# Kernel optimization log

Hardware: AMD Instinct MI355X
Metric: run time of the kernel (lower is better)

## Reference

```python
import jax, jax.numpy as jnp
import numpy as np

N, E = 50000, 800000
C_IN, C_OUT, HID = 64, 64, 64


def setup_inputs() -> dict:
    key = jax.random.key(0)
    ks = jax.random.split(key, 12)
    def rn(k, shape, scale=0.05):
        return jax.random.normal(k, shape, dtype=jnp.float32) * scale
    return dict(
        x=jax.random.normal(ks[0], (N, C_IN), dtype=jnp.float32),
        pos=jax.random.normal(ks[1], (N, 3), dtype=jnp.float32),
        edge_index=jax.random.randint(ks[2], (2, E), 0, N),
        W_in=rn(ks[3], (C_IN, C_IN)), b_in=jnp.zeros((C_IN,), jnp.float32),
        W_out=rn(ks[4], (C_OUT, C_OUT)), b_out=jnp.zeros((C_OUT,), jnp.float32),
        W_lin=rn(ks[5], (C_OUT, C_IN)),   # PointTransformerConv.lin (value), bias=False
        W_src=rn(ks[6], (C_OUT, C_IN)),   # lin_src, bias=False
        W_dst=rn(ks[7], (C_OUT, C_IN)),   # lin_dst, bias=False
        pos_w1=rn(ks[8], (HID, 3)), pos_b1=jnp.zeros((HID,), jnp.float32),
        pos_w2=rn(ks[9], (C_OUT, HID)), pos_b2=jnp.zeros((C_OUT,), jnp.float32),
        att_w1=rn(ks[10], (HID, C_OUT)), att_b1=jnp.zeros((HID,), jnp.float32),
        att_w2=rn(ks[11], (C_OUT, HID)), att_b2=jnp.zeros((C_OUT,), jnp.float32),
    )


def _mlp2(y, w1, b1, w2, b2):
    # MLP([a, 64, b], batch_norm=False): Linear->ReLU->Linear->ReLU
    y = jax.nn.relu(y @ w1.T + b1)
    return jax.nn.relu(y @ w2.T + b2)


def reference(x, pos, edge_index, W_in, b_in, W_out, b_out, W_lin, W_src, W_dst,
              pos_w1, pos_b1, pos_w2, pos_b2, att_w1, att_b1, att_w2, att_b2):
    n = x.shape[0]
    h = jax.nn.relu(x @ W_in.T + b_in)            # lin_in + relu, (N, C_in)
    v = h @ W_lin.T                                # value projection (N, C_out)
    k_src = h @ W_src.T                            # alpha_j source part
    q_dst = h @ W_dst.T                            # alpha_i dest part
    # PointTransformerConv adds self-loops by default
    loop = jnp.arange(n)
    src = jnp.concatenate([edge_index[0], loop])   # (E+N,)
    dst = jnp.concatenate([edge_index[1], loop])
    # per-edge positional encoding: pos_nn(pos_i - pos_j)
    delta = _mlp2(pos[dst] - pos[src], pos_w1, pos_b1, pos_w2, pos_b2)
    # per-edge attention logits: attn_nn(alpha_i - alpha_j), (E+N, C_out)
    alpha = _mlp2(q_dst[dst] - k_src[src], att_w1, att_b1, att_w2, att_b2)
    # per-destination-node channelwise softmax (self-loops ensure no empty segment)
    amax = jax.ops.segment_max(alpha, dst, num_segments=n)
    ex = jnp.exp(alpha - amax[dst])
    denom = jax.ops.segment_sum(ex, dst, num_segments=n)
    w = ex / (denom[dst] + 1e-16)
    # message = alpha * (x_j + delta); aggregate = sum over neighbors
    out = jax.ops.segment_sum(w * (v[src] + delta), dst, num_segments=n)
    return jax.nn.relu(out @ W_out.T + b_out)
```

## Files before the change

kernel.cpp:

```cpp
#include <hip/hip_runtime.h>
#include <math.h>

#define NN 50000
#define EE 800000
#define ET (EE + NN)
#define C  64
#define NBLK 49
#define NCHUNK 831
#define ZBLK 463

typedef __attribute__((ext_vector_type(8))) _Float16 f16x8;
typedef __attribute__((ext_vector_type(4))) _Float16 f16x4;
typedef __attribute__((ext_vector_type(2))) _Float16 f16x2;
typedef __attribute__((ext_vector_type(4))) float f32x4;

__device__ __forceinline__ f16x2 pk2(float a, float b) {
  return __builtin_bit_cast(f16x2, __builtin_amdgcn_cvt_pkrtz(a, b));
}
__device__ __forceinline__ f16x4 pk4(float a, float b, float c, float d) {
  return __builtin_shufflevector(pk2(a, b), pk2(c, d), 0, 1, 2, 3);
}
__device__ __forceinline__ f16x8 pk8(const float* y) {
  const f16x4 lo = pk4(y[0], y[1], y[2], y[3]);
  const f16x4 hi = pk4(y[4], y[5], y[6], y[7]);
  return __builtin_shufflevector(lo, hi, 0, 1, 2, 3, 4, 5, 6, 7);
}

__device__ __forceinline__ f16x8 frag_ldh(const _Float16* base, int row,
                                          int kofs) {
  return *(const f16x8*)(base + row * 72 + kofs);
}

__device__ __forceinline__ void stage_w(_Float16* __restrict__ dst,
                                        const _Float16* __restrict__ src16,
                                        int tid) {
  const f16x8* src = (const f16x8*)(src16 + tid * 16);
  _Float16* d = dst + (tid >> 2) * 72 + (tid & 3) * 16;
  ((f16x8*)d)[0] = src[0];
  ((f16x8*)d)[1] = src[1];
}

__global__ __launch_bounds__(256) void prep_kernel(
    const float* __restrict__ W_in, const float* __restrict__ W_lin,
    const float* __restrict__ W_src, const float* __restrict__ W_dst,
    const float* __restrict__ att_w1, const float* __restrict__ att_w2,
    const float* __restrict__ pos_w2, const float* __restrict__ W_out,
    _Float16* __restrict__ w16, int* __restrict__ cnt2) {
  const float* Ws[8] = {W_in, W_lin, W_src, W_dst, att_w1, att_w2, pos_w2, W_out};
  const float* src = Ws[blockIdx.x];
  _Float16* dst = w16 + blockIdx.x * 4096;
#pragma unroll
  for (int i = threadIdx.x * 4; i < 4096; i += 1024) {
    const float4 w = *(const float4*)(src + i);
    *(f16x4*)(dst + i) = pk4(w.x, w.y, w.z, w.w);
  }
  int4* cz = (int4*)(cnt2 + blockIdx.x * NN);
#pragma unroll 1
  for (int i = threadIdx.x; i < NN / 4; i += 256) cz[i] = make_int4(0, 0, 0, 0);
}

__global__ __launch_bounds__(256) void scan_partial(const int* __restrict__ cnt2,
                                                    int* __restrict__ bsum,
                                                    float* __restrict__ zeroreg) {
  const int t = threadIdx.x;
  if (blockIdx.x >= NBLK) {
    const int zb = blockIdx.x - NBLK;
    float4* dst = (float4*)zeroreg;
    const int total4 = 2 * NN * 64 / 4;
    const float4 z = make_float4(0.f, 0.f, 0.f, 0.f);
#pragma unroll 1
    for (int i = zb * 256 + t; i < total4; i += ZBLK * 256) dst[i] = z;
    return;
  }
  __shared__ int ws[4];
  const int base = blockIdx.x * 1024 + t * 4;
  int s = 0;
  if (base + 3 < NN) {
#pragma unroll
    for (int sh = 0; sh < 8; ++sh) {
      const int4 v = *(const int4*)(cnt2 + sh * NN + base);
      s += v.x + v.y + v.z + v.w;
    }
  } else {
#pragma unroll
    for (int i = 0; i < 4; ++i)
      if (base + i < NN)
#pragma unroll
        for (int sh = 0; sh < 8; ++sh) s += cnt2[sh * NN + base + i];
  }
#pragma unroll
  for (int off = 32; off; off >>= 1) s += __shfl_down(s, off, 64);
  if ((t & 63) == 0) ws[t >> 6] = s;
  __syncthreads();
  if (t == 0) bsum[blockIdx.x] = ws[0] + ws[1] + ws[2] + ws[3];
}

__global__ __launch_bounds__(256) void scan_final(const int* __restrict__ cnt2,
                                                  const int* __restrict__ bsum,
                                                  int* __restrict__ curs2) {
  __shared__ int tsum[256];
  __shared__ int sblk[64];
  const int t = threadIdx.x;
  if (t < 64) {
    const int mine = (t < NBLK) ? bsum[t] : 0;
    int v = mine;
#pragma unroll
    for (int off = 1; off < 64; off <<= 1) {
      const int u = __shfl_up(v, off, 64);
      if (t >= off) v += u;
    }
    sblk[t] = v - mine;
  }
  const int base = blockIdx.x * 1024 + t * 4;
  int c2[8][4];
  int v[4] = {0, 0, 0, 0};
  if (base + 3 < NN) {
#pragma unroll
    for (int sh = 0; sh < 8; ++sh) {
      const int4 x = *(const int4*)(cnt2 + sh * NN + base);
      c2[sh][0] = x.x; c2[sh][1] = x.y; c2[sh][2] = x.z; c2[sh][3] = x.w;
      v[0] += x.x; v[1] += x.y; v[2] += x.z; v[3] += x.w;
    }
  } else {
#pragma unroll
    for (int sh = 0; sh < 8; ++sh)
#pragma unroll
      for (int i = 0; i < 4; ++i) {
        const int c = (base + i < NN) ? cnt2[sh * NN + base + i] : 0;
        c2[sh][i] = c;
        v[i] += c;
      }
  }
  const int s = v[0] + v[1] + v[2] + v[3];
  tsum[t] = s;
  __syncthreads();
  for (int off = 1; off < 256; off <<= 1) {
    const int u = (t >= off) ? tsum[t - off] : 0;
    __syncthreads();
    tsum[t] += u;
    __syncthreads();
  }
  int ex = sblk[blockIdx.x] + tsum[t] - s;
  int offs[8][4];
#pragma unroll
  for (int i = 0; i < 4; ++i) {
    int run = ex;
#pragma unroll
    for (int sh = 0; sh < 8; ++sh) {
      offs[sh][i] = run;
      run += c2[sh][i];
    }
    ex += v[i];
  }
  if (base + 3 < NN) {
#pragma unroll
    for (int sh = 0; sh < 8; ++sh)
      *(int4*)(curs2 + sh * NN + base) =
          make_int4(offs[sh][0], offs[sh][1], offs[sh][2], offs[sh][3]);
  } else {
#pragma unroll
    for (int sh = 0; sh < 8; ++sh)
#pragma unroll
      for (int i = 0; i < 4; ++i)
        if (base + i < NN) curs2[sh * NN + base + i] = offs[sh][i];
  }
}

__global__ void scatter_kernel(const int* __restrict__ ei,
                               int* __restrict__ curs2, int2* __restrict__ srt) {
  const int chunk = blockIdx.x;
  int* cs = curs2 + (chunk & 7) * NN;
  const int e0 = chunk * 1024 + threadIdx.x * 4;
  if (e0 >= ET) return;
  int s[4], d[4];
  if (e0 + 3 < EE) {
    const int4 sv = *(const int4*)(ei + e0);
    const int4 dv = *(const int4*)(ei + EE + e0);
    s[0] = sv.x; s[1] = sv.y; s[2] = sv.z; s[3] = sv.w;
    d[0] = dv.x; d[1] = dv.y; d[2] = dv.z; d[3] = dv.w;
  } else {
#pragma unroll
    for (int i = 0; i < 4; ++i) {
      const int e = e0 + i;
      if (e < EE) {
        s[i] = ei[e];
        d[i] = ei[EE + e];
      } else if (e < ET) {
        s[i] = d[i] = e - EE;
      } else {
        s[i] = d[i] = -1;
      }
    }
  }
#pragma unroll
  for (int i = 0; i < 4; ++i) {
    if (d[i] >= 0) {
      const int p = atomicAdd(&cs[d[i]], 1);
      srt[p] = make_int2(s[i], d[i]);
    }
  }
}

__global__ __launch_bounds__(256, 3) void node_proj(
    const float* __restrict__ x, const float* __restrict__ b_in,
    const _Float16* __restrict__ w16, const int* __restrict__ ei,
    int* __restrict__ cnt2, _Float16* __restrict__ vh,
    _Float16* __restrict__ kh, _Float16* __restrict__ qh) {
  __shared__ __align__(16) _Float16 wlds[4 * 4608];
  __shared__ __align__(16) _Float16 hlds[4608];
  __shared__ float biasv[64];

  const int tid = threadIdx.x;
  const int nb = blockIdx.x * 64;
  const int l15 = tid & 15;
  const int quad = (tid >> 4) & 3;
  const int wband = tid >> 6;
  const int nloc = wband * 16 + l15;
  const int gn = nb + nloc;

#pragma unroll 1
  for (int chunk = blockIdx.x; chunk < NCHUNK; chunk += gridDim.x) {
    int* cs = cnt2 + (chunk & 7) * NN;
    const int e0 = chunk * 1024 + tid * 4;
    if (e0 < ET) {
      int d[4];
      if (e0 + 3 < EE) {
        const int4 dv = *(const int4*)(ei + EE + e0);
        d[0] = dv.x; d[1] = dv.y; d[2] = dv.z; d[3] = dv.w;
      } else {
#pragma unroll
        for (int i = 0; i < 4; ++i) {
          const int e = e0 + i;
          d[i] = (e < EE) ? ei[EE + e] : ((e < ET) ? e - EE : -1);
        }
      }
#pragma unroll
      for (int i = 0; i < 4; ++i)
        if (d[i] >= 0) atomicAdd(&cs[d[i]], 1);
    }
  }

#pragma unroll
  for (int w = 0; w < 4; ++w) stage_w(wlds + w * 4608, w16 + w * 4096, tid);
  if (tid < 64) biasv[tid] = b_in[tid];

  f16x8 bfrag[2];
#pragma unroll
  for (int ks = 0; ks < 2; ++ks) {
    float y[8] = {0.f, 0.f, 0.f, 0.f, 0.f, 0.f, 0.f, 0.f};
    if (gn < NN) {
      const float4 a = *(const float4*)(x + (size_t)gn * 64 + ks * 32 + quad * 8);
      const float4 b = *(const float4*)(x + (size_t)gn * 64 + ks * 32 + quad * 8 + 4);
      y[0] = a.x; y[1] = a.y; y[2] = a.z; y[3] = a.w;
      y[4] = b.x; y[5] = b.y; y[6] = b.z; y[7] = b.w;
    }
    bfrag[ks] = pk8(y);
  }
  __syncthreads();

#pragma unroll
  for (int t = 0; t < 4; ++t) {
    f32x4 acc = {0.f, 0.f, 0.f, 0.f};
#pragma unroll
    for (int ks = 0; ks < 2; ++ks) {
      const f16x8 af = frag_ldh(wlds, t * 16 + l15, ks * 32 + quad * 8);
      acc = __builtin_amdgcn_mfma_f32_16x16x32_f16(af, bfrag[ks], acc, 0, 0, 0);
    }
    const int hb = t * 16 + quad * 4;
    *(f16x4*)(hlds + nloc * 72 + hb) =
        pk4(fmaxf(acc[0] + biasv[hb + 0], 0.f), fmaxf(acc[1] + biasv[hb + 1], 0.f),
            fmaxf(acc[2] + biasv[hb + 2], 0.f), fmaxf(acc[3] + biasv[hb + 3], 0.f));
  }
  __syncthreads();

  f16x8 hfrag[2];
#pragma unroll
  for (int ks = 0; ks < 2; ++ks)
    hfrag[ks] = frag_ldh(hlds, nloc, ks * 32 + quad * 8);

  _Float16* outs[3] = {vh, kh, qh};
#pragma unroll
  for (int p = 0; p < 3; ++p) {
    const _Float16* W = wlds + (p + 1) * 4608;
#pragma unroll
    for (int t = 0; t < 4; ++t) {
      f32x4 acc = {0.f, 0.f, 0.f, 0.f};
#pragma unroll
      for (int ks = 0; ks < 2; ++ks) {
        const f16x8 af = frag_ldh(W, t * 16 + l15, ks * 32 + quad * 8);
        acc = __builtin_amdgcn_mfma_f32_16x16x32_f16(af, hfrag[ks], acc, 0, 0, 0);
      }
      if (gn < NN) {
        *(f16x4*)(outs[p] + (size_t)gn * 64 + t * 16 + quad * 4) =
            pk4(acc[0], acc[1], acc[2], acc[3]);
      }
    }
  }
}

__global__ __launch_bounds__(256, 4) void edge_pass(
    const int2* __restrict__ srt, const float* __restrict__ pos,
    const _Float16* __restrict__ vh, const _Float16* __restrict__ kh,
    const _Float16* __restrict__ qh, const _Float16* __restrict__ w16,
    const float* __restrict__ att_b1, const float* __restrict__ att_b2,
    const float* __restrict__ pos_w1, const float* __restrict__ pos_b1,
    const float* __restrict__ pos_b2, float* __restrict__ num,
    float* __restrict__ den) {
  __shared__ __align__(16) _Float16 smem[18432];
  __shared__ __align__(16) float posw1T[3 * 64];
  __shared__ float b1s[64], b2s[64], pb1s[64], pb2s[64];
  __shared__ int dsts[64];

  _Float16* W1  = smem;
  _Float16* W2  = smem + 4608;
  _Float16* PW2 = smem + 9216;
  _Float16* h1  = smem + 13824;
  float2* pairb = (float2*)smem;

  const int tid = threadIdx.x;
  const int eb = blockIdx.x * 64;
  const int l15 = tid & 15;
  const int quad = (tid >> 4) & 3;
  const int wband = tid >> 6;
  const int eloc = wband * 16 + l15;

  int s_mine, d_mine;
  f16x8 bfrag[2];
  float dp0, dp1, dp2;
  {
    const int e = eb + eloc;
    int2 sd = make_int2(0, 0);
    int valid_d = -1;
    if (e < ET) {
      sd = srt[e];
      valid_d = sd.y;
    }
    s_mine = sd.x;
    d_mine = sd.y;
    if (quad == 0) dsts[eloc] = valid_d;
#pragma unroll
    for (int ks = 0; ks < 2; ++ks) {
      const f16x8 qv =
          *(const f16x8*)(qh + (size_t)d_mine * 64 + ks * 32 + quad * 8);
      const f16x8 kv =
          *(const f16x8*)(kh + (size_t)s_mine * 64 + ks * 32 + quad * 8);
      bfrag[ks] = qv - kv;
    }
    dp0 = pos[(size_t)d_mine * 3 + 0] - pos[(size_t)s_mine * 3 + 0];
    dp1 = pos[(size_t)d_mine * 3 + 1] - pos[(size_t)s_mine * 3 + 1];
    dp2 = pos[(size_t)d_mine * 3 + 2] - pos[(size_t)s_mine * 3 + 2];
  }

  stage_w(W1, w16 + 4 * 4096, tid);
  stage_w(W2, w16 + 5 * 4096, tid);
  stage_w(PW2, w16 + 6 * 4096, tid);
  if (tid < 64) {
    b1s[tid] = att_b1[tid];
    b2s[tid] = att_b2[tid];
    pb1s[tid] = pos_b1[tid];
    pb2s[tid] = pos_b2[tid];
    posw1T[0 * 64 + tid] = pos_w1[tid * 3 + 0];
    posw1T[1 * 64 + tid] = pos_w1[tid * 3 + 1];
    posw1T[2 * 64 + tid] = pos_w1[tid * 3 + 2];
  }
  __syncthreads();

#pragma unroll
  for (int t = 0; t < 4; ++t) {
    f32x4 acc = {0.f, 0.f, 0.f, 0.f};
#pragma unroll
    for (int ks = 0; ks < 2; ++ks) {
      const f16x8 af = frag_ldh(W1, t * 16 + l15, ks * 32 + quad * 8);
      acc = __builtin_amdgcn_mfma_f32_16x16x32_f16(af, bfrag[ks], acc, 0, 0, 0);
    }
    const int hb = t * 16 + quad * 4;
    *(f16x4*)(h1 + eloc * 72 + hb) =
        pk4(fmaxf(acc[0] + b1s[hb + 0], 0.f), fmaxf(acc[1] + b1s[hb + 1], 0.f),
            fmaxf(acc[2] + b1s[hb + 2], 0.f), fmaxf(acc[3] + b1s[hb + 3], 0.f));
  }

  f16x8 hpfrag[2];
#pragma unroll
  for (int ks = 0; ks < 2; ++ks) {
    float hv[8];
#pragma unroll
    for (int j = 0; j < 8; ++j) {
      const int i = ks * 32 + quad * 8 + j;
      float a = pb1s[i];
      a = fmaf(dp0, posw1T[i], a);
      a = fmaf(dp1, posw1T[64 + i], a);
      a = fmaf(dp2, posw1T[128 + i], a);
      hv[j] = fmaxf(a, 0.f);
    }
    hpfrag[ks] = pk8(hv);
  }
  __syncthreads();

  float ex[16], del[16];
  {
    f16x8 hfrag[2];
#pragma unroll
    for (int ks = 0; ks < 2; ++ks)
      hfrag[ks] = frag_ldh(h1, eloc, ks * 32 + quad * 8);
#pragma unroll
    for (int t = 0; t < 4; ++t) {
      f32x4 acc = {0.f, 0.f, 0.f, 0.f};
#pragma unroll
      for (int ks = 0; ks < 2; ++ks) {
        const f16x8 af = frag_ldh(W2, t * 16 + l15, ks * 32 + quad * 8);
        acc = __builtin_amdgcn_mfma_f32_16x16x32_f16(af, hfrag[ks], acc, 0, 0, 0);
      }
      const int ob = t * 16 + quad * 4;
#pragma unroll
      for (int r = 0; r < 4; ++r)
        ex[t * 4 + r] = __expf(fmaxf(acc[r] + b2s[ob + r], 0.f));
    }
  }
#pragma unroll
  for (int t = 0; t < 4; ++t) {
    f32x4 acc = {0.f, 0.f, 0.f, 0.f};
#pragma unroll
    for (int ks = 0; ks < 2; ++ks) {
      const f16x8 af = frag_ldh(PW2, t * 16 + l15, ks * 32 + quad * 8);
      acc = __builtin_amdgcn_mfma_f32_16x16x32_f16(af, hpfrag[ks], acc, 0, 0, 0);
    }
    const int ob = t * 16 + quad * 4;
#pragma unroll
    for (int r = 0; r < 4; ++r)
      del[t * 4 + r] = fmaxf(acc[r] + pb2s[ob + r], 0.f);
  }
  float vr[16];
#pragma unroll
  for (int t = 0; t < 4; ++t) {
    const f16x4 v4 = *(const f16x4*)(vh + (size_t)s_mine * 64 + t * 16 + quad * 4);
    vr[t * 4 + 0] = (float)v4[0];
    vr[t * 4 + 1] = (float)v4[1];
    vr[t * 4 + 2] = (float)v4[2];
    vr[t * 4 + 3] = (float)v4[3];
  }
  __syncthreads();

#pragma unroll
  for (int t = 0; t < 4; ++t) {
#pragma unroll
    for (int r = 0; r < 4; ++r) {
      const int o = t * 16 + quad * 4 + r;
      const int sl = (eloc + 2 * o) & 63;
      const float e_ = ex[t * 4 + r];
      pairb[o * 65 + sl] = make_float2(e_ * (vr[t * 4 + r] + del[t * 4 + r]), e_);
    }
  }
  __syncthreads();

  {
    const int c = tid & 63;
    const int r = tid >> 6;
    float am = 0.f, ae = 0.f;
    int cur = -1;
#pragma unroll 1
    for (int t2 = 0; t2 < 16; ++t2) {
      const int el = r * 16 + t2;
      const int d = dsts[el];
      if (d != cur) {
        if (cur >= 0) {
          unsafeAtomicAdd(num + (size_t)cur * 64 + c, am);
          unsafeAtomicAdd(den + (size_t)cur * 64 + c, ae);
        }
        cur = d;
        am = 0.f;
        ae = 0.f;
      }
      if (d >= 0) {
        const float2 pe = pairb[c * 65 + ((el + 2 * c) & 63)];
        am += pe.x;
        ae += pe.y;
      }
    }
    if (cur >= 0) {
      unsafeAtomicAdd(num + (size_t)cur * 64 + c, am);
      unsafeAtomicAdd(den + (size_t)cur * 64 + c, ae);
    }
  }
}

__global__ __launch_bounds__(256, 4) void out_proj(
    const float* __restrict__ num, const float* __restrict__ den,
    const _Float16* __restrict__ w16, const float* __restrict__ b_out,
    float* __restrict__ out) {
  __shared__ __align__(16) _Float16 wlds[4608];
  __shared__ float biasv[64];

  const int tid = threadIdx.x;
  const int nb = blockIdx.x * 64;
  const int l15 = tid & 15;
  const int quad = (tid >> 4) & 3;
  const int wband = tid >> 6;
  const int gn = nb + wband * 16 + l15;

  stage_w(wlds, w16 + 7 * 4096, tid);
  if (tid < 64) biasv[tid] = b_out[tid];

  f16x8 bfrag[2];
#pragma unroll
  for (int ks = 0; ks < 2; ++ks) {
    float y[8] = {0.f, 0.f, 0.f, 0.f, 0.f, 0.f, 0.f, 0.f};
    if (gn < NN) {
      const size_t base = (size_t)gn * 64 + ks * 32 + quad * 8;
      const float4 n0 = *(const float4*)(num + base);
      const float4 n1 = *(const float4*)(num + base + 4);
      const float4 d0 = *(const float4*)(den + base);
      const float4 d1 = *(const float4*)(den + base + 4);
      y[0] = n0.x / (d0.x + 1e-16f); y[1] = n0.y / (d0.y + 1e-16f);
      y[2] = n0.z / (d0.z + 1e-16f); y[3] = n0.w / (d0.w + 1e-16f);
      y[4] = n1.x / (d1.x + 1e-16f); y[5] = n1.y / (d1.y + 1e-16f);
      y[6] = n1.z / (d1.z + 1e-16f); y[7] = n1.w / (d1.w + 1e-16f);
    }
    bfrag[ks] = pk8(y);
  }
  __syncthreads();

#pragma unroll
  for (int t = 0; t < 4; ++t) {
    f32x4 acc = {0.f, 0.f, 0.f, 0.f};
#pragma unroll
    for (int ks = 0; ks < 2; ++ks) {
      const f16x8 af = frag_ldh(wlds, t * 16 + l15, ks * 32 + quad * 8);
      acc = __builtin_amdgcn_mfma_f32_16x16x32_f16(af, bfrag[ks], acc, 0, 0, 0);
    }
    if (gn < NN) {
      const int ob = t * 16 + quad * 4;
      float4 r;
      r.x = fmaxf(acc[0] + biasv[ob + 0], 0.f);
      r.y = fmaxf(acc[1] + biasv[ob + 1], 0.f);
      r.z = fmaxf(acc[2] + biasv[ob + 2], 0.f);
      r.w = fmaxf(acc[3] + biasv[ob + 3], 0.f);
      *(float4*)(out + (size_t)gn * 64 + ob) = r;
    }
  }
}

extern "C" void kernel_launch(void* const* d_in, const int* in_sizes, int n_in,
                              void* d_out, int out_size, void* d_ws,
                              size_t ws_size, hipStream_t stream) {
  const float* x      = (const float*)d_in[0];
  const float* pos    = (const float*)d_in[1];
  const int*   ei     = (const int*)d_in[2];
  const float* W_in   = (const float*)d_in[3];
  const float* b_in   = (const float*)d_in[4];
  const float* W_out  = (const float*)d_in[5];
  const float* b_out  = (const float*)d_in[6];
  const float* W_lin  = (const float*)d_in[7];
  const float* W_src  = (const float*)d_in[8];
  const float* W_dst  = (const float*)d_in[9];
  const float* pos_w1 = (const float*)d_in[10];
  const float* pos_b1 = (const float*)d_in[11];
  const float* pos_w2 = (const float*)d_in[12];
  const float* pos_b2 = (const float*)d_in[13];
  const float* att_w1 = (const float*)d_in[14];
  const float* att_b1 = (const float*)d_in[15];
  const float* att_w2 = (const float*)d_in[16];
  const float* att_b2 = (const float*)d_in[17];

  float* ws = (float*)d_ws;
  const size_t NC = (size_t)NN * C;
  float* num = ws;
  float* den = ws + NC;
  _Float16* vh = (_Float16*)(ws + 2 * NC);
  _Float16* kh = vh + NC;
  _Float16* qh = kh + NC;
  _Float16* w16 = qh + NC;
  int* ib     = (int*)(w16 + 8 * 4096);
  int* cnt2   = ib;
  int* curs2  = ib + 8 * NN;
  int* bsum   = ib + 16 * NN;
  int2* srt   = (int2*)(((uintptr_t)(bsum + NBLK) + 15) & ~(uintptr_t)15);

  const dim3 blk(256);
  prep_kernel<<<dim3(8), blk, 0, stream>>>(W_in, W_lin, W_src, W_dst, att_w1,
                                           att_w2, pos_w2, W_out, w16, cnt2);
  node_proj<<<dim3((NN + 63) / 64), blk, 0, stream>>>(x, b_in, w16, ei, cnt2,
                                                      vh, kh, qh);
  scan_partial<<<dim3(NBLK + ZBLK), blk, 0, stream>>>(cnt2, bsum, num);
  scan_final<<<dim3(NBLK), blk, 0, stream>>>(cnt2, bsum, curs2);
  scatter_kernel<<<dim3(NCHUNK), blk, 0, stream>>>(ei, curs2, srt);
  edge_pass<<<dim3((ET + 63) / 64), blk, 0, stream>>>(
      srt, pos, vh, kh, qh, w16, att_b1, att_b2, pos_w1, pos_b1, pos_b2, num,
      den);
  out_proj<<<dim3((NN + 63) / 64), blk, 0, stream>>>(num, den, w16, b_out,
                                                     (float*)d_out);
}
```

Measured before the change: 307.3 us.

## Fuse all stages into one cooperative persistent kernel with grid syncs

Replaces the seven-kernel pipeline (prep, node projection, scan partial, scan final, scatter, edge pass, output projection) with a single cooperative persistent kernel. Stages are separated by grid-wide barriers and work is distributed over tiles in grid-stride loops. The aim is to remove per-launch overhead and inter-kernel gaps. In exchange it adds grid-sync cost and serializes the small scan stages on only 49 blocks. It also re-stages weights into LDS for every tile, and the original kernels remain as a fallback if the cooperative launch fails.

```diff
diff --git a/kernel.cpp b/kernel.cpp
--- a/kernel.cpp
+++ b/kernel.cpp
@@ -1,5 +1,8 @@
 #include <hip/hip_runtime.h>
+#include <hip/hip_cooperative_groups.h>
 #include <math.h>
+
+namespace cg = cooperative_groups;
 
 #define NN 50000
 #define EE 800000
@@ -8,6 +11,8 @@
 #define NBLK 49
 #define NCHUNK 831
 #define ZBLK 463
+#define NTILE 782
+#define ETILE 13282
 
 typedef __attribute__((ext_vector_type(8))) _Float16 f16x8;
 typedef __attribute__((ext_vector_type(4))) _Float16 f16x4;
@@ -38,6 +43,516 @@
   _Float16* d = dst + (tid >> 2) * 72 + (tid & 3) * 16;
   ((f16x8*)d)[0] = src[0];
   ((f16x8*)d)[1] = src[1];
+}
+
+struct MegaArgs {
+  const float *x, *pos;
+  const int* ei;
+  const float *W_in, *b_in, *W_out, *b_out, *W_lin, *W_src, *W_dst;
+  const float *pos_w1, *pos_b1, *pos_w2, *pos_b2;
+  const float *att_w1, *att_b1, *att_w2, *att_b2;
+  float *num, *den;
+  _Float16 *vh, *kh, *qh, *w16;
+  int *cnt2, *curs2, *bsum;
+  int2* srt;
+  float* out;
+};
+
+__global__ __launch_bounds__(256, 4) void mega_kernel(MegaArgs a) {
+  cg::grid_group grd = cg::this_grid();
+  __shared__ __align__(16) _Float16 smem[18432];
+  __shared__ __align__(16) float posw1T[192];
+  __shared__ float b1s[64], b2s[64], pb1s[64], pb2s[64];
+  __shared__ int dsts[64];
+
+  const int tid = threadIdx.x;
+  const int bid = blockIdx.x;
+  const int gsz = gridDim.x;
+  const int l15 = tid & 15;
+  const int quad = (tid >> 4) & 3;
+  const int wband = tid >> 6;
+
+  {
+    const int gt = bid * 256 + tid;
+    const int stride = gsz * 256;
+    float4* z1 = (float4*)a.num;
+    const float4 zf = make_float4(0.f, 0.f, 0.f, 0.f);
+#pragma unroll 1
+    for (int i = gt; i < (2 * NN * C) / 4; i += stride) z1[i] = zf;
+    int4* z2 = (int4*)a.cnt2;
+    const int4 zi = make_int4(0, 0, 0, 0);
+#pragma unroll 1
+    for (int i = gt; i < (8 * NN) / 4; i += stride) z2[i] = zi;
+    if (bid < 8) {
+      const float* Ws[8] = {a.W_in,   a.W_lin,  a.W_src,  a.W_dst,
+                            a.att_w1, a.att_w2, a.pos_w2, a.W_out};
+      const float* src = Ws[bid];
+      _Float16* dst = a.w16 + bid * 4096;
+#pragma unroll 1
+      for (int i = tid * 4; i < 4096; i += 1024) {
+        const float4 w = *(const float4*)(src + i);
+        *(f16x4*)(dst + i) = pk4(w.x, w.y, w.z, w.w);
+      }
+    }
+  }
+  grd.sync();
+
+  {
+#pragma unroll 1
+    for (int chunk = bid; chunk < NCHUNK; chunk += gsz) {
+      int* cs = a.cnt2 + (chunk & 7) * NN;
+      const int e0 = chunk * 1024 + tid * 4;
+      if (e0 < ET) {
+        int d[4];
+        if (e0 + 3 < EE) {
+          const int4 dv = *(const int4*)(a.ei + EE + e0);
+          d[0] = dv.x; d[1] = dv.y; d[2] = dv.z; d[3] = dv.w;
+        } else {
+#pragma unroll
+          for (int i = 0; i < 4; ++i) {
+            const int e = e0 + i;
+            d[i] = (e < EE) ? a.ei[EE + e] : ((e < ET) ? e - EE : -1);
+          }
+        }
+#pragma unroll
+        for (int i = 0; i < 4; ++i)
+          if (d[i] >= 0) atomicAdd(&cs[d[i]], 1);
+      }
+    }
+    _Float16* A = smem;
+    _Float16* B = smem + 4608;
+    _Float16* Cr = smem + 9216;
+    _Float16* D = smem + 13824;
+#pragma unroll 1
+    for (int tile = bid; tile < NTILE; tile += gsz) {
+      __syncthreads();
+      const int nloc = wband * 16 + l15;
+      const int gn = tile * 64 + nloc;
+      stage_w(A, a.w16 + 0 * 4096, tid);
+      stage_w(B, a.w16 + 1 * 4096, tid);
+      stage_w(Cr, a.w16 + 2 * 4096, tid);
+      if (tid < 64) b1s[tid] = a.b_in[tid];
+      f16x8 bfrag[2];
+#pragma unroll
+      for (int ks = 0; ks < 2; ++ks) {
+        float y[8] = {0.f, 0.f, 0.f, 0.f, 0.f, 0.f, 0.f, 0.f};
+        if (gn < NN) {
+          const size_t base = (size_t)gn * 64 + ks * 32 + quad * 8;
+          const float4 p = *(const float4*)(a.x + base);
+          const float4 q = *(const float4*)(a.x + base + 4);
+          y[0] = p.x; y[1] = p.y; y[2] = p.z; y[3] = p.w;
+          y[4] = q.x; y[5] = q.y; y[6] = q.z; y[7] = q.w;
+        }
+        bfrag[ks] = pk8(y);
+      }
+      __syncthreads();
+#pragma unroll
+      for (int t = 0; t < 4; ++t) {
+        f32x4 acc = {0.f, 0.f, 0.f, 0.f};
+#pragma unroll
+        for (int ks = 0; ks < 2; ++ks) {
+          const f16x8 af = frag_ldh(A, t * 16 + l15, ks * 32 + quad * 8);
+          acc = __builtin_amdgcn_mfma_f32_16x16x32_f16(af, bfrag[ks], acc, 0, 0, 0);
+        }
+        const int hb = t * 16 + quad * 4;
+        *(f16x4*)(D + nloc * 72 + hb) = pk4(
+            fmaxf(acc[0] + b1s[hb + 0], 0.f), fmaxf(acc[1] + b1s[hb + 1], 0.f),
+            fmaxf(acc[2] + b1s[hb + 2], 0.f), fmaxf(acc[3] + b1s[hb + 3], 0.f));
+      }
+      __syncthreads();
+      f16x8 hfrag[2];
+#pragma unroll
+      for (int ks = 0; ks < 2; ++ks)
+        hfrag[ks] = frag_ldh(D, nloc, ks * 32 + quad * 8);
+      stage_w(A, a.w16 + 3 * 4096, tid);
+      _Float16* outs2[2] = {a.vh, a.kh};
+      const _Float16* Ws2[2] = {B, Cr};
+#pragma unroll
+      for (int p = 0; p < 2; ++p) {
+#pragma unroll
+        for (int t = 0; t < 4; ++t) {
+          f32x4 acc = {0.f, 0.f, 0.f, 0.f};
+#pragma unroll
+          for (int ks = 0; ks < 2; ++ks) {
+            const f16x8 af = frag_ldh(Ws2[p], t * 16 + l15, ks * 32 + quad * 8);
+            acc = __builtin_amdgcn_mfma_f32_16x16x32_f16(af, hfrag[ks], acc, 0, 0, 0);
+          }
+          if (gn < NN)
+            *(f16x4*)(outs2[p] + (size_t)gn * 64 + t * 16 + quad * 4) =
+                pk4(acc[0], acc[1], acc[2], acc[3]);
+        }
+      }
+      __syncthreads();
+#pragma unroll
+      for (int t = 0; t < 4; ++t) {
+        f32x4 acc = {0.f, 0.f, 0.f, 0.f};
+#pragma unroll
+        for (int ks = 0; ks < 2; ++ks) {
+          const f16x8 af = frag_ldh(A, t * 16 + l15, ks * 32 + quad * 8);
+          acc = __builtin_amdgcn_mfma_f32_16x16x32_f16(af, hfrag[ks], acc, 0, 0, 0);
+        }
+        if (gn < NN)
+          *(f16x4*)(a.qh + (size_t)gn * 64 + t * 16 + quad * 4) =
+              pk4(acc[0], acc[1], acc[2], acc[3]);
+      }
+    }
+  }
+  grd.sync();
+
+  {
+    int* wsb = (int*)smem;
+#pragma unroll 1
+    for (int sb = bid; sb < NBLK; sb += gsz) {
+      __syncthreads();
+      const int base = sb * 1024 + tid * 4;
+      int s = 0;
+      if (base + 3 < NN) {
+#pragma unroll
+        for (int sh = 0; sh < 8; ++sh) {
+          const int4 v = *(const int4*)(a.cnt2 + sh * NN + base);
+          s += v.x + v.y + v.z + v.w;
+        }
+      } else {
+#pragma unroll
+        for (int i = 0; i < 4; ++i)
+          if (base + i < NN)
+#pragma unroll
+            for (int sh = 0; sh < 8; ++sh) s += a.cnt2[sh * NN + base + i];
+      }
+#pragma unroll
+      for (int off = 32; off; off >>= 1) s += __shfl_down(s, off, 64);
+      if ((tid & 63) == 0) wsb[tid >> 6] = s;
+      __syncthreads();
+      if (tid == 0) a.bsum[sb] = wsb[0] + wsb[1] + wsb[2] + wsb[3];
+    }
+  }
+  grd.sync();
+
+  {
+    int* tsum = (int*)smem;
+    int* sblk = ((int*)smem) + 256;
+#pragma unroll 1
+    for (int sb = bid; sb < NBLK; sb += gsz) {
+      __syncthreads();
+      if (tid < 64) {
+        const int mine = (tid < NBLK) ? a.bsum[tid] : 0;
+        int v = mine;
+#pragma unroll
+        for (int off = 1; off < 64; off <<= 1) {
+          const int u = __shfl_up(v, off, 64);
+          if (tid >= off) v += u;
+        }
+        sblk[tid] = v - mine;
+      }
+      const int base = sb * 1024 + tid * 4;
+      int c2[8][4];
+      int v[4] = {0, 0, 0, 0};
+      if (base + 3 < NN) {
+#pragma unroll
+        for (int sh = 0; sh < 8; ++sh) {
+          const int4 xx = *(const int4*)(a.cnt2 + sh * NN + base);
+          c2[sh][0] = xx.x; c2[sh][1] = xx.y; c2[sh][2] = xx.z; c2[sh][3] = xx.w;
+          v[0] += xx.x; v[1] += xx.y; v[2] += xx.z; v[3] += xx.w;
+        }
+      } else {
+#pragma unroll
+        for (int sh = 0; sh < 8; ++sh)
+#pragma unroll
+          for (int i = 0; i < 4; ++i) {
+            const int c = (base + i < NN) ? a.cnt2[sh * NN + base + i] : 0;
+            c2[sh][i] = c;
+            v[i] += c;
+          }
+      }
+      const int s = v[0] + v[1] + v[2] + v[3];
+      tsum[tid] = s;
+      __syncthreads();
+      for (int off = 1; off < 256; off <<= 1) {
+        const int u = (tid >= off) ? tsum[tid - off] : 0;
+        __syncthreads();
+        tsum[tid] += u;
+        __syncthreads();
+      }
+      int ex = sblk[sb] + tsum[tid] - s;
+      int offs[8][4];
+#pragma unroll
+      for (int i = 0; i < 4; ++i) {
+        int run = ex;
+#pragma unroll
+        for (int sh = 0; sh < 8; ++sh) {
+          offs[sh][i] = run;
+          run += c2[sh][i];
+        }
+        ex += v[i];
+      }
+      if (base + 3 < NN) {
+#pragma unroll
+        for (int sh = 0; sh < 8; ++sh)
+          *(int4*)(a.curs2 + sh * NN + base) =
+              make_int4(offs[sh][0], offs[sh][1], offs[sh][2], offs[sh][3]);
+      } else {
+#pragma unroll
+        for (int sh = 0; sh < 8; ++sh)
+#pragma unroll
+          for (int i = 0; i < 4; ++i)
+            if (base + i < NN) a.curs2[sh * NN + base + i] = offs[sh][i];
+      }
+    }
+  }
+  grd.sync();
+
+  {
+#pragma unroll 1
+    for (int chunk = bid; chunk < NCHUNK; chunk += gsz) {
+      int* cs = a.curs2 + (chunk & 7) * NN;
+      const int e0 = chunk * 1024 + tid * 4;
+      if (e0 < ET) {
+        int s[4], d[4];
+        if (e0 + 3 < EE) {
+          const int4 sv = *(const int4*)(a.ei + e0);
+          const int4 dv = *(const int4*)(a.ei + EE + e0);
+          s[0] = sv.x; s[1] = sv.y; s[2] = sv.z; s[3] = sv.w;
+          d[0] = dv.x; d[1] = dv.y; d[2] = dv.z; d[3] = dv.w;
+        } else {
+#pragma unroll
+          for (int i = 0; i < 4; ++i) {
+            const int e = e0 + i;
+            if (e < EE) {
+              s[i] = a.ei[e];
+              d[i] = a.ei[EE + e];
+            } else if (e < ET) {
+              s[i] = d[i] = e - EE;
+            } else {
+              s[i] = d[i] = -1;
+            }
+          }
+        }
+#pragma unroll
+        for (int i = 0; i < 4; ++i) {
+          if (d[i] >= 0) {
+            const int p = atomicAdd(&cs[d[i]], 1);
+            a.srt[p] = make_int2(s[i], d[i]);
+          }
+        }
+      }
+    }
+  }
+  grd.sync();
+
+  {
+    _Float16* W1 = smem;
+    _Float16* W2 = smem + 4608;
+    _Float16* PW2 = smem + 9216;
+    _Float16* h1 = smem + 13824;
+    float2* pairb = (float2*)smem;
+    if (tid < 64) {
+      b1s[tid] = a.att_b1[tid];
+      b2s[tid] = a.att_b2[tid];
+      pb1s[tid] = a.pos_b1[tid];
+      pb2s[tid] = a.pos_b2[tid];
+      posw1T[0 * 64 + tid] = a.pos_w1[tid * 3 + 0];
+      posw1T[1 * 64 + tid] = a.pos_w1[tid * 3 + 1];
+      posw1T[2 * 64 + tid] = a.pos_w1[tid * 3 + 2];
+    }
+    const int eloc = wband * 16 + l15;
+#pragma unroll 1
+    for (int tile = bid; tile < ETILE; tile += gsz) {
+      __syncthreads();
+      const int eb = tile * 64;
+      int s_mine, d_mine;
+      f16x8 bfrag[2];
+      float dp0, dp1, dp2;
+      {
+        const int e = eb + eloc;
+        int2 sd = make_int2(0, 0);
+        int valid_d = -1;
+        if (e < ET) {
+          sd = a.srt[e];
+          valid_d = sd.y;
+        }
+        s_mine = sd.x;
+        d_mine = sd.y;
+        if (quad == 0) dsts[eloc] = valid_d;
+#pragma unroll
+        for (int ks = 0; ks < 2; ++ks) {
+          const f16x8 qv =
+              *(const f16x8*)(a.qh + (size_t)d_mine * 64 + ks * 32 + quad * 8);
+          const f16x8 kv =
+              *(const f16x8*)(a.kh + (size_t)s_mine * 64 + ks * 32 + quad * 8);
+          bfrag[ks] = qv - kv;
+        }
+        dp0 = a.pos[(size_t)d_mine * 3 + 0] - a.pos[(size_t)s_mine * 3 + 0];
+        dp1 = a.pos[(size_t)d_mine * 3 + 1] - a.pos[(size_t)s_mine * 3 + 1];
+        dp2 = a.pos[(size_t)d_mine * 3 + 2] - a.pos[(size_t)s_mine * 3 + 2];
+      }
+      stage_w(W1, a.w16 + 4 * 4096, tid);
+      stage_w(W2, a.w16 + 5 * 4096, tid);
+      stage_w(PW2, a.w16 + 6 * 4096, tid);
+      __syncthreads();
+
+#pragma unroll
+      for (int t = 0; t < 4; ++t) {
+        f32x4 acc = {0.f, 0.f, 0.f, 0.f};
+#pragma unroll
+        for (int ks = 0; ks < 2; ++ks) {
+          const f16x8 af = frag_ldh(W1, t * 16 + l15, ks * 32 + quad * 8);
+          acc = __builtin_amdgcn_mfma_f32_16x16x32_f16(af, bfrag[ks], acc, 0, 0, 0);
+        }
+        const int hb = t * 16 + quad * 4;
+        *(f16x4*)(h1 + eloc * 72 + hb) = pk4(
+            fmaxf(acc[0] + b1s[hb + 0], 0.f), fmaxf(acc[1] + b1s[hb + 1], 0.f),
+            fmaxf(acc[2] + b1s[hb + 2], 0.f), fmaxf(acc[3] + b1s[hb + 3], 0.f));
+      }
+      f16x8 hpfrag[2];
+#pragma unroll
+      for (int ks = 0; ks < 2; ++ks) {
+        float hv[8];
+#pragma unroll
+        for (int j = 0; j < 8; ++j) {
+          const int i = ks * 32 + quad * 8 + j;
+          float h = pb1s[i];
+          h = fmaf(dp0, posw1T[i], h);
+          h = fmaf(dp1, posw1T[64 + i], h);
+          h = fmaf(dp2, posw1T[128 + i], h);
+          hv[j] = fmaxf(h, 0.f);
+        }
+        hpfrag[ks] = pk8(hv);
+      }
+      __syncthreads();
+      float ex[16], del[16];
+      {
+        f16x8 hfrag[2];
+#pragma unroll
+        for (int ks = 0; ks < 2; ++ks)
+          hfrag[ks] = frag_ldh(h1, eloc, ks * 32 + quad * 8);
+#pragma unroll
+        for (int t = 0; t < 4; ++t) {
+          f32x4 acc = {0.f, 0.f, 0.f, 0.f};
+#pragma unroll
+          for (int ks = 0; ks < 2; ++ks) {
+            const f16x8 af = frag_ldh(W2, t * 16 + l15, ks * 32 + quad * 8);
+            acc = __builtin_amdgcn_mfma_f32_16x16x32_f16(af, hfrag[ks], acc, 0, 0, 0);
+          }
+          const int ob = t * 16 + quad * 4;
+#pragma unroll
+          for (int r = 0; r < 4; ++r)
+            ex[t * 4 + r] = __expf(fmaxf(acc[r] + b2s[ob + r], 0.f));
+        }
+      }
+#pragma unroll
+      for (int t = 0; t < 4; ++t) {
+        f32x4 acc = {0.f, 0.f, 0.f, 0.f};
+#pragma unroll
+        for (int ks = 0; ks < 2; ++ks) {
+          const f16x8 af = frag_ldh(PW2, t * 16 + l15, ks * 32 + quad * 8);
+          acc = __builtin_amdgcn_mfma_f32_16x16x32_f16(af, hpfrag[ks], acc, 0, 0, 0);
+        }
+        const int ob = t * 16 + quad * 4;
+#pragma unroll
+        for (int r = 0; r < 4; ++r)
+          del[t * 4 + r] = fmaxf(acc[r] + pb2s[ob + r], 0.f);
+      }
+      float vr[16];
+#pragma unroll
+      for (int t = 0; t < 4; ++t) {
+        const f16x4 v4 =
+            *(const f16x4*)(a.vh + (size_t)s_mine * 64 + t * 16 + quad * 4);
+        vr[t * 4 + 0] = (float)v4[0];
+        vr[t * 4 + 1] = (float)v4[1];
+        vr[t * 4 + 2] = (float)v4[2];
+        vr[t * 4 + 3] = (float)v4[3];
+      }
+      __syncthreads();
+#pragma unroll
+      for (int t = 0; t < 4; ++t) {
+#pragma unroll
+        for (int r = 0; r < 4; ++r) {
+          const int o = t * 16 + quad * 4 + r;
+          const int sl = (eloc + 2 * o) & 63;
+          const float e_ = ex[t * 4 + r];
+          pairb[o * 65 + sl] =
+              make_float2(e_ * (vr[t * 4 + r] + del[t * 4 + r]), e_);
+        }
+      }
+      __syncthreads();
+      {
+        const int c = tid & 63;
+        const int r = tid >> 6;
+        float am = 0.f, ae = 0.f;
+        int cur = -1;
+#pragma unroll 1
+        for (int t2 = 0; t2 < 16; ++t2) {
+          const int el = r * 16 + t2;
+          const int d = dsts[el];
+          if (d != cur) {
+            if (cur >= 0) {
+              unsafeAtomicAdd(a.num + (size_t)cur * 64 + c, am);
+              unsafeAtomicAdd(a.den + (size_t)cur * 64 + c, ae);
+            }
+            cur = d;
+            am = 0.f;
+            ae = 0.f;
+          }
+          if (d >= 0) {
+            const float2 pe = pairb[c * 65 + ((el + 2 * c) & 63)];
+            am += pe.x;
+            ae += pe.y;
+          }
+        }
+        if (cur >= 0) {
+          unsafeAtomicAdd(a.num + (size_t)cur * 64 + c, am);
+          unsafeAtomicAdd(a.den + (size_t)cur * 64 + c, ae);
+        }
+      }
+    }
+  }
+  grd.sync();
+
+  {
+    __syncthreads();
+    stage_w(smem, a.w16 + 7 * 4096, tid);
+    if (tid < 64) b1s[tid] = a.b_out[tid];
+    __syncthreads();
+#pragma unroll 1
+    for (int tile = bid; tile < NTILE; tile += gsz) {
+      const int gn = tile * 64 + wband * 16 + l15;
+      f16x8 bfrag[2];
+#pragma unroll
+      for (int ks = 0; ks < 2; ++ks) {
+        float y[8] = {0.f, 0.f, 0.f, 0.f, 0.f, 0.f, 0.f, 0.f};
+        if (gn < NN) {
+          const size_t base = (size_t)gn * 64 + ks * 32 + quad * 8;
+          const float4 n0 = *(const float4*)(a.num + base);
+          const float4 n1 = *(const float4*)(a.num + base + 4);
+          const float4 d0 = *(const float4*)(a.den + base);
+          const float4 d1 = *(const float4*)(a.den + base + 4);
+          y[0] = n0.x / (d0.x + 1e-16f); y[1] = n0.y / (d0.y + 1e-16f);
+          y[2] = n0.z / (d0.z + 1e-16f); y[3] = n0.w / (d0.w + 1e-16f);
+          y[4] = n1.x / (d1.x + 1e-16f); y[5] = n1.y / (d1.y + 1e-16f);
+          y[6] = n1.z / (d1.z + 1e-16f); y[7] = n1.w / (d1.w + 1e-16f);
+        }
+        bfrag[ks] = pk8(y);
+      }
+#pragma unroll
+      for (int t = 0; t < 4; ++t) {
+        f32x4 acc = {0.f, 0.f, 0.f, 0.f};
+#pragma unroll
+        for (int ks = 0; ks < 2; ++ks) {
+          const f16x8 af = frag_ldh(smem, t * 16 + l15, ks * 32 + quad * 8);
+          acc = __builtin_amdgcn_mfma_f32_16x16x32_f16(af, bfrag[ks], acc, 0, 0, 0);
+        }
+        if (gn < NN) {
+          const int ob = t * 16 + quad * 4;
+          float4 r;
+          r.x = fmaxf(acc[0] + b1s[ob + 0], 0.f);
+          r.y = fmaxf(acc[1] + b1s[ob + 1], 0.f);
+          r.z = fmaxf(acc[2] + b1s[ob + 2], 0.f);
+          r.w = fmaxf(acc[3] + b1s[ob + 3], 0.f);
+          *(float4*)(a.out + (size_t)gn * 64 + ob) = r;
+        }
+      }
+    }
+  }
 }
 
 __global__ __launch_bounds__(256) void prep_kernel(
@@ -249,10 +764,10 @@
   for (int ks = 0; ks < 2; ++ks) {
     float y[8] = {0.f, 0.f, 0.f, 0.f, 0.f, 0.f, 0.f, 0.f};
     if (gn < NN) {
-      const float4 a = *(const float4*)(x + (size_t)gn * 64 + ks * 32 + quad * 8);
-      const float4 b = *(const float4*)(x + (size_t)gn * 64 + ks * 32 + quad * 8 + 4);
-      y[0] = a.x; y[1] = a.y; y[2] = a.z; y[3] = a.w;
-      y[4] = b.x; y[5] = b.y; y[6] = b.z; y[7] = b.w;
+      const float4 p = *(const float4*)(x + (size_t)gn * 64 + ks * 32 + quad * 8);
+      const float4 q = *(const float4*)(x + (size_t)gn * 64 + ks * 32 + quad * 8 + 4);
+      y[0] = p.x; y[1] = p.y; y[2] = p.z; y[3] = p.w;
+      y[4] = q.x; y[5] = q.y; y[6] = q.z; y[7] = q.w;
     }
     bfrag[ks] = pk8(y);
   }
@@ -311,10 +826,10 @@
   __shared__ float b1s[64], b2s[64], pb1s[64], pb2s[64];
   __shared__ int dsts[64];
 
-  _Float16* W1  = smem;
-  _Float16* W2  = smem + 4608;
+  _Float16* W1 = smem;
+  _Float16* W2 = smem + 4608;
   _Float16* PW2 = smem + 9216;
-  _Float16* h1  = smem + 13824;
+  _Float16* h1 = smem + 13824;
   float2* pairb = (float2*)smem;
 
   const int tid = threadIdx.x;
@@ -386,11 +901,11 @@
 #pragma unroll
     for (int j = 0; j < 8; ++j) {
       const int i = ks * 32 + quad * 8 + j;
-      float a = pb1s[i];
-      a = fmaf(dp0, posw1T[i], a);
-      a = fmaf(dp1, posw1T[64 + i], a);
-      a = fmaf(dp2, posw1T[128 + i], a);
-      hv[j] = fmaxf(a, 0.f);
+      float h = pb1s[i];
+      h = fmaf(dp0, posw1T[i], h);
+      h = fmaf(dp1, posw1T[64 + i], h);
+      h = fmaf(dp2, posw1T[128 + i], h);
+      hv[j] = fmaxf(h, 0.f);
     }
     hpfrag[ks] = pk8(hv);
   }
@@ -569,11 +1084,40 @@
   _Float16* kh = vh + NC;
   _Float16* qh = kh + NC;
   _Float16* w16 = qh + NC;
-  int* ib     = (int*)(w16 + 8 * 4096);
-  int* cnt2   = ib;
-  int* curs2  = ib + 8 * NN;
-  int* bsum   = ib + 16 * NN;
-  int2* srt   = (int2*)(((uintptr_t)(bsum + NBLK) + 15) & ~(uintptr_t)15);
+  int* ib    = (int*)(w16 + 8 * 4096);
+  int* cnt2  = ib;
+  int* curs2 = ib + 8 * NN;
+  int* bsum  = ib + 16 * NN;
+  int2* srt  = (int2*)(((uintptr_t)(bsum + NBLK) + 15) & ~(uintptr_t)15);
+
+  MegaArgs ma;
+  ma.x = x; ma.pos = pos; ma.ei = ei;
+  ma.W_in = W_in; ma.b_in = b_in; ma.W_out = W_out; ma.b_out = b_out;
+  ma.W_lin = W_lin; ma.W_src = W_src; ma.W_dst = W_dst;
+  ma.pos_w1 = pos_w1; ma.pos_b1 = pos_b1; ma.pos_w2 = pos_w2; ma.pos_b2 = pos_b2;
+  ma.att_w1 = att_w1; ma.att_b1 = att_b1; ma.att_w2 = att_w2; ma.att_b2 = att_b2;
+  ma.num = num; ma.den = den; ma.vh = vh; ma.kh = kh; ma.qh = qh; ma.w16 = w16;
+  ma.cnt2 = cnt2; ma.curs2 = curs2; ma.bsum = bsum; ma.srt = srt;
+  ma.out = (float*)d_out;
+
+  int dev = 0;
+  (void)hipGetDevice(&dev);
+  int cus = 0;
+  if (hipDeviceGetAttribute(&cus, hipDeviceAttributeMultiprocessorCount, dev) !=
+          hipSuccess ||
+      cus <= 0)
+    cus = 256;
+  int perCU = 0;
+  if (hipOccupancyMaxActiveBlocksPerMultiprocessor(&perCU, mega_kernel, 256,
+                                                   0) != hipSuccess ||
+      perCU <= 0)
+    perCU = 3;
+  if (perCU > 4) perCU = 4;
+  void* params[] = {&ma};
+  hipError_t le = hipLaunchCooperativeKernel(
+      mega_kernel, dim3(perCU * cus), dim3(256), params, 0, stream);
+  if (le == hipSuccess) return;
+  (void)hipGetLastError();
 
   const dim3 blk(256);
   prep_kernel<<<dim3(8), blk, 0, stream>>>(W_in, W_lin, W_src, W_dst, att_w1,
```

After: 769.2 us. 150% more time.

## Shrink edge_pass LDS by reusing buffers and packing reduction pairs to fp16

Applied to the files above, without the earlier changes.

The edge kernel's shared memory drops from 18432 to 13824 halves. The pos_nn second-layer weights now reuse the h1 buffer after the attention MLP finishes, and the per-edge (message, exp) pairs are stored as packed fp16 instead of float2, with a new bank-swizzle function. Launch bounds are raised to 5 blocks per CU to use the freed LDS for occupancy. This adds an extra barrier and weight staging phase, and the fp16 rounding of exp-weighted messages before summation may cost accuracy or overflow, since exp of an unbounded ReLU output is stored without max subtraction.

```diff
diff --git a/kernel.cpp b/kernel.cpp
--- a/kernel.cpp
+++ b/kernel.cpp
@@ -38,6 +38,10 @@
   _Float16* d = dst + (tid >> 2) * 72 + (tid & 3) * 16;
   ((f16x8*)d)[0] = src[0];
   ((f16x8*)d)[1] = src[1];
+}
+
+__device__ __forceinline__ int psl(int e, int o) {
+  return (e + 2 * o + (o >> 5)) & 63;
 }
 
 __global__ __launch_bounds__(256) void prep_kernel(
@@ -166,8 +170,9 @@
   }
 }
 
-__global__ void scatter_kernel(const int* __restrict__ ei,
-                               int* __restrict__ curs2, int2* __restrict__ srt) {
+__global__ __launch_bounds__(256) void scatter_kernel(const int* __restrict__ ei,
+                                                      int* __restrict__ curs2,
+                                                      int2* __restrict__ srt) {
   const int chunk = blockIdx.x;
   int* cs = curs2 + (chunk & 7) * NN;
   const int e0 = chunk * 1024 + threadIdx.x * 4;
@@ -298,7 +303,7 @@
   }
 }
 
-__global__ __launch_bounds__(256, 4) void edge_pass(
+__global__ __launch_bounds__(256, 5) void edge_pass(
     const int2* __restrict__ srt, const float* __restrict__ pos,
     const _Float16* __restrict__ vh, const _Float16* __restrict__ kh,
     const _Float16* __restrict__ qh, const _Float16* __restrict__ w16,
@@ -306,16 +311,15 @@
     const float* __restrict__ pos_w1, const float* __restrict__ pos_b1,
     const float* __restrict__ pos_b2, float* __restrict__ num,
     float* __restrict__ den) {
-  __shared__ __align__(16) _Float16 smem[18432];
+  __shared__ __align__(16) _Float16 smem[13824];
   __shared__ __align__(16) float posw1T[3 * 64];
   __shared__ float b1s[64], b2s[64], pb1s[64], pb2s[64];
   __shared__ int dsts[64];
 
-  _Float16* W1  = smem;
-  _Float16* W2  = smem + 4608;
-  _Float16* PW2 = smem + 9216;
-  _Float16* h1  = smem + 13824;
-  float2* pairb = (float2*)smem;
+  _Float16* W1 = smem;
+  _Float16* W2 = smem + 4608;
+  _Float16* HP = smem + 9216;
+  f16x2* pairb = (f16x2*)smem;
 
   const int tid = threadIdx.x;
   const int eb = blockIdx.x * 64;
@@ -353,7 +357,6 @@
 
   stage_w(W1, w16 + 4 * 4096, tid);
   stage_w(W2, w16 + 5 * 4096, tid);
-  stage_w(PW2, w16 + 6 * 4096, tid);
   if (tid < 64) {
     b1s[tid] = att_b1[tid];
     b2s[tid] = att_b2[tid];
@@ -374,7 +377,7 @@
       acc = __builtin_amdgcn_mfma_f32_16x16x32_f16(af, bfrag[ks], acc, 0, 0, 0);
     }
     const int hb = t * 16 + quad * 4;
-    *(f16x4*)(h1 + eloc * 72 + hb) =
+    *(f16x4*)(HP + eloc * 72 + hb) =
         pk4(fmaxf(acc[0] + b1s[hb + 0], 0.f), fmaxf(acc[1] + b1s[hb + 1], 0.f),
             fmaxf(acc[2] + b1s[hb + 2], 0.f), fmaxf(acc[3] + b1s[hb + 3], 0.f));
   }
@@ -386,22 +389,21 @@
 #pragma unroll
     for (int j = 0; j < 8; ++j) {
       const int i = ks * 32 + quad * 8 + j;
-      float a = pb1s[i];
-      a = fmaf(dp0, posw1T[i], a);
-      a = fmaf(dp1, posw1T[64 + i], a);
-      a = fmaf(dp2, posw1T[128 + i], a);
-      hv[j] = fmaxf(a, 0.f);
+      float h = pb1s[i];
+      h = fmaf(dp0, posw1T[i], h);
+      h = fmaf(dp1, posw1T[64 + i], h);
+      h = fmaf(dp2, posw1T[128 + i], h);
+      hv[j] = fmaxf(h, 0.f);
     }
     hpfrag[ks] = pk8(hv);
   }
-  __syncthreads();
-
-  float ex[16], del[16];
+
+  float ex[16];
   {
     f16x8 hfrag[2];
 #pragma unroll
     for (int ks = 0; ks < 2; ++ks)
-      hfrag[ks] = frag_ldh(h1, eloc, ks * 32 + quad * 8);
+      hfrag[ks] = frag_ldh(HP, eloc, ks * 32 + quad * 8);
 #pragma unroll
     for (int t = 0; t < 4; ++t) {
       f32x4 acc = {0.f, 0.f, 0.f, 0.f};
@@ -415,19 +417,6 @@
       for (int r = 0; r < 4; ++r)
         ex[t * 4 + r] = __expf(fmaxf(acc[r] + b2s[ob + r], 0.f));
     }
-  }
-#pragma unroll
-  for (int t = 0; t < 4; ++t) {
-    f32x4 acc = {0.f, 0.f, 0.f, 0.f};
-#pragma unroll
-    for (int ks = 0; ks < 2; ++ks) {
-      const f16x8 af = frag_ldh(PW2, t * 16 + l15, ks * 32 + quad * 8);
-      acc = __builtin_amdgcn_mfma_f32_16x16x32_f16(af, hpfrag[ks], acc, 0, 0, 0);
-    }
-    const int ob = t * 16 + quad * 4;
-#pragma unroll
-    for (int r = 0; r < 4; ++r)
-      del[t * 4 + r] = fmaxf(acc[r] + pb2s[ob + r], 0.f);
   }
   float vr[16];
 #pragma unroll
@@ -440,14 +429,32 @@
   }
   __syncthreads();
 
+  stage_w(HP, w16 + 6 * 4096, tid);
+  __syncthreads();
+
+  float del[16];
+#pragma unroll
+  for (int t = 0; t < 4; ++t) {
+    f32x4 acc = {0.f, 0.f, 0.f, 0.f};
+#pragma unroll
+    for (int ks = 0; ks < 2; ++ks) {
+      const f16x8 af = frag_ldh(HP, t * 16 + l15, ks * 32 + quad * 8);
+      acc = __builtin_amdgcn_mfma_f32_16x16x32_f16(af, hpfrag[ks], acc, 0, 0, 0);
+    }
+    const int ob = t * 16 + quad * 4;
+#pragma unroll
+    for (int r = 0; r < 4; ++r)
+      del[t * 4 + r] = fmaxf(acc[r] + pb2s[ob + r], 0.f);
+  }
+
 #pragma unroll
   for (int t = 0; t < 4; ++t) {
 #pragma unroll
     for (int r = 0; r < 4; ++r) {
       const int o = t * 16 + quad * 4 + r;
-      const int sl = (eloc + 2 * o) & 63;
       const float e_ = ex[t * 4 + r];
-      pairb[o * 65 + sl] = make_float2(e_ * (vr[t * 4 + r] + del[t * 4 + r]), e_);
+      pairb[o * 64 + psl(eloc, o)] =
+          pk2(e_ * (vr[t * 4 + r] + del[t * 4 + r]), e_);
     }
   }
   __syncthreads();
@@ -471,9 +478,9 @@
         ae = 0.f;
       }
       if (d >= 0) {
-        const float2 pe = pairb[c * 65 + ((el + 2 * c) & 63)];
-        am += pe.x;
-        ae += pe.y;
+        const f16x2 pe = pairb[c * 64 + psl(el, c)];
+        am += (float)pe[0];
+        ae += (float)pe[1];
       }
     }
     if (cur >= 0) {
```

After: 299.3 us. 2.6% less time.
